# Kernel tuning notes

Measured on AMD Instinct MI355X. Metric: run time of the kernel, lower is better.

## Reference

```python
import jax, jax.numpy as jnp
import numpy as np

EPS = 1e-5


def layer_norm(x, g, b):
    m = jnp.mean(x, axis=-1, keepdims=True)
    v = jnp.mean((x - m) ** 2, axis=-1, keepdims=True)
    return (x - m) / jnp.sqrt(v + EPS) * g + b


def rel_shift(x, klen):
    # x: [q, p, b, n] -> Transformer-XL relative shift -> [q, klen, b, n]
    q, p, b, n = x.shape
    x = jnp.reshape(x, (p, q, b, n))
    x = x[1:]
    x = jnp.reshape(x, (q, p - 1, b, n))
    return x[:, :klen]


def setup_inputs() -> dict:
    S, B, D, NH, DH, DF = 1024, 4, 1024, 16, 64, 4096
    key = jax.random.key(0)
    ks = jax.random.split(key, 16)
    w = 0.02  # scale random params for numerical sanity
    return {
        "src": jax.random.normal(ks[0], (S, B, D), jnp.float32),
        "pos_emb": jax.random.normal(ks[1], (S + 1, B, D), jnp.float32),
        "src_mask": jnp.zeros((S, S), dtype=bool),
        "qw": jax.random.normal(ks[2], (D, NH, DH), jnp.float32) * w,
        "kw": jax.random.normal(ks[3], (D, NH, DH), jnp.float32) * w,
        "vw": jax.random.normal(ks[4], (D, NH, DH), jnp.float32) * w,
        "rw": jax.random.normal(ks[5], (D, NH, DH), jnp.float32) * w,
        "ow": jax.random.normal(ks[6], (D, NH, DH), jnp.float32) * w,
        "r_w_bias": jax.random.normal(ks[7], (NH, DH), jnp.float32) * w,
        "r_r_bias": jax.random.normal(ks[8], (NH, DH), jnp.float32) * w,
        "w1": jax.random.normal(ks[9], (DF, D), jnp.float32) * w,
        "b1": jnp.zeros((DF,), jnp.float32),
        "w2": jax.random.normal(ks[10], (D, DF), jnp.float32) * w,
        "b2": jnp.zeros((D,), jnp.float32),
        "g1": jnp.ones((D,), jnp.float32),
        "beta1": jnp.zeros((D,), jnp.float32),
        "g2": jnp.ones((D,), jnp.float32),
        "beta2": jnp.zeros((D,), jnp.float32),
    }


def reference(src, pos_emb, src_mask, qw, kw, vw, rw, ow, r_w_bias, r_r_bias,
              w1, b1, w2, b2, g1, beta1, g2, beta2):
    S = src.shape[0]
    d_head = qw.shape[-1]
    scale = 1.0 / d_head ** 0.5

    # mem=None -> cat == src; dropout layers are identity (eval)
    q_head = jnp.einsum('ibh,hnd->ibnd', src, qw)
    k_head = jnp.einsum('ibh,hnd->ibnd', src, kw)
    v_head = jnp.einsum('ibh,hnd->ibnd', src, vw)
    k_pos = jnp.einsum('ibh,hnd->ibnd', pos_emb, rw)

    ac = jnp.einsum('ibnd,jbnd->ijbn', q_head + r_w_bias, k_head)       # [S,S,B,N]
    bd = jnp.einsum('ibnd,jbnd->ijbn', q_head + r_r_bias, k_pos)        # [S,S+1,B,N]
    bd = rel_shift(bd, klen=S)

    mask = src_mask.astype(ac.dtype)[:, :, None, None]
    attn_score = (ac + bd) * scale - 1e30 * mask
    attn_prob = jax.nn.softmax(attn_score, axis=1)

    attn_vec = jnp.einsum('ijbn,jbnd->ibnd', attn_prob, v_head)
    attn_out = jnp.einsum('ibnd,hnd->ibh', attn_vec, ow)

    x = layer_norm(src + attn_out, g1, beta1)
    ff = jax.nn.gelu(x @ w1.T + b1, approximate=False) @ w2.T + b2
    return layer_norm(x + ff, g2, beta2)
```

## Files before the change

### kernel.cpp

```cpp
#include <hip/hip_runtime.h>
#include <math.h>

typedef __bf16 bf16x8 __attribute__((ext_vector_type(8)));
typedef __bf16 bf16x4 __attribute__((ext_vector_type(4)));
typedef float f32x4 __attribute__((ext_vector_type(4)));

__device__ __forceinline__ void gload_lds16(const __bf16* g, __bf16* l) {
  __builtin_amdgcn_global_load_lds((const __attribute__((address_space(1))) void*)g,
                                   (__attribute__((address_space(3))) void*)l, 16, 0, 0);
}

__device__ __forceinline__ float gelu_exact(float v) {
  return 0.5f * v * (1.f + erff(v * 0.70710678118654752f));
}

__global__ __launch_bounds__(256) void prep_all(
    const float* __restrict__ src, __bf16* __restrict__ srcB2,
    const float* __restrict__ pos, __bf16* __restrict__ posB,
    const float* __restrict__ ow, __bf16* __restrict__ owB,
    const float* __restrict__ w1, __bf16* __restrict__ w1B,
    const float* __restrict__ w2, __bf16* __restrict__ w2B,
    const float* __restrict__ qw, const float* __restrict__ kw,
    const float* __restrict__ vw, const float* __restrict__ rw,
    __bf16* __restrict__ qkvT, __bf16* __restrict__ rwT) {
  __shared__ float t[32][33];
  int bid = blockIdx.x;
  const int tid = threadIdx.x;
  if (bid < 4096) {
    const int i = bid & 1023, b = bid >> 10;
    const float4 v = *(const float4*)(src + ((size_t)(i * 4 + b)) * 1024 + tid * 4);
    bf16x4 o = {(__bf16)v.x, (__bf16)v.y, (__bf16)v.z, (__bf16)v.w};
    *(bf16x4*)(srcB2 + (size_t)bid * 1024 + tid * 4) = o;
    return;
  }
  bid -= 4096;
  if (bid < 3329) {
    const float* in; __bf16* out;
    if (bid < 1025) { in = pos; out = posB; }
    else if (bid < 1281) { bid -= 1025; in = ow; out = owB; }
    else if (bid < 2305) { bid -= 1281; in = w1; out = w1B; }
    else { bid -= 2305; in = w2; out = w2B; }
    const int base = bid * 4096 + tid * 4;
#pragma unroll
    for (int k2 = 0; k2 < 4; ++k2) {
      const int off = base + k2 * 1024;
      float4 v = *(const float4*)(in + off);
      bf16x4 o = {(__bf16)v.x, (__bf16)v.y, (__bf16)v.z, (__bf16)v.w};
      *(bf16x4*)(out + off) = o;
    }
    return;
  }
  bid -= 3329;
  const int z = bid >> 10, rem = bid & 1023;
  const float* in; __bf16* out;
  switch (z) {
    case 0: in = qw; out = qkvT; break;
    case 1: in = kw; out = qkvT + 1024 * 1024; break;
    case 2: in = vw; out = qkvT + 2048 * 1024; break;
    default: in = rw; out = rwT; break;
  }
  const int c0 = (rem & 31) * 32, r0 = (rem >> 5) * 32;
  const int tx = tid & 31, ty = tid >> 5;
  for (int yy = ty; yy < 32; yy += 8)
    t[yy][tx] = in[(size_t)(r0 + yy) * 1024 + c0 + tx];
  __syncthreads();
  for (int yy = ty; yy < 32; yy += 8)
    out[(size_t)(c0 + yy) * 1024 + r0 + tx] = (__bf16)t[tx][yy];
}

template<int BM, int BN, int MODE>
__device__ __forceinline__ void gemm_body(
    const __bf16* __restrict__ A, const __bf16* __restrict__ BT,
    float* __restrict__ Cf, __bf16* __restrict__ Cb,
    const float* __restrict__ bias, int M, int N, int K,
    int kStart, int kChunk, int mBase, int nBase, char* smemRaw) {
  constexpr int BK = 32;
  constexpr int ALOAD = (BM * BK) / 2048;
  constexpr int BLOAD = (BN * BK) / 2048;
  __bf16* lA = (__bf16*)smemRaw;
  __bf16* lB = (__bf16*)(smemRaw + 4 * BM * BK);
  const int tid = threadIdx.x;
  const int w = tid >> 6, l = tid & 63;
  const int lr = l & 15, lk = l >> 4;
  const int srow = tid >> 2;
  const int scol = (tid & 3) * 8;
  const int wbase = w * 512;

  const __bf16* aSrc[ALOAD];
  const __bf16* bSrc[BLOAD];
#pragma unroll
  for (int i = 0; i < ALOAD; ++i) {
    int grow = mBase + srow + i * 64;
    grow = grow < M ? grow : M - 1;
    aSrc[i] = A + (size_t)grow * K + kStart + scol;
  }
#pragma unroll
  for (int i = 0; i < BLOAD; ++i) {
    const int grow = nBase + srow + i * 64;
    bSrc[i] = BT + (size_t)grow * K + kStart + scol;
  }
  auto stage = [&](int buf) {
#pragma unroll
    for (int i = 0; i < ALOAD; ++i) {
      gload_lds16(aSrc[i], &lA[buf * BM * BK + i * 2048 + wbase]);
      aSrc[i] += BK;
    }
#pragma unroll
    for (int i = 0; i < BLOAD; ++i) {
      gload_lds16(bSrc[i], &lB[buf * BN * BK + i * 2048 + wbase]);
      bSrc[i] += BK;
    }
  };

  constexpr int WM = BM / 2, WN = BN / 2;
  constexpr int MF = WM / 16, NF = WN / 16;
  const int wr = w >> 1, wc = w & 1;
  f32x4 acc[MF][NF] = {};

  const int nIter = kChunk / BK;
  stage(0);
  int cur = 0;
#pragma unroll 1
  for (int t = 0; t < nIter; ++t) {
    __syncthreads();
    if (t + 1 < nIter) stage(cur ^ 1);
    bf16x8 af[MF], bfr[NF];
#pragma unroll
    for (int mi = 0; mi < MF; ++mi)
      af[mi] = *(const bf16x8*)&lA[cur * BM * BK + (wr * WM + mi * 16 + lr) * BK + lk * 8];
#pragma unroll
    for (int nj = 0; nj < NF; ++nj)
      bfr[nj] = *(const bf16x8*)&lB[cur * BN * BK + (wc * WN + nj * 16 + lr) * BK + lk * 8];
#pragma unroll
    for (int mi = 0; mi < MF; ++mi)
#pragma unroll
      for (int nj = 0; nj < NF; ++nj)
        acc[mi][nj] = __builtin_amdgcn_mfma_f32_16x16x32_bf16(af[mi], bfr[nj], acc[mi][nj], 0, 0, 0);
    cur ^= 1;
  }
#pragma unroll
  for (int mi = 0; mi < MF; ++mi) {
#pragma unroll
    for (int nj = 0; nj < NF; ++nj) {
      const int col = nBase + wc * WN + nj * 16 + lr;
      const int row0 = mBase + wr * WM + mi * 16 + lk * 4;
#pragma unroll
      for (int j = 0; j < 4; ++j) {
        const int row = row0 + j;
        if (row < M) {
          float v = acc[mi][nj][j];
          if constexpr (MODE == 1) {
            v = gelu_exact(v + bias[col]);
            Cb[(size_t)row * N + col] = (__bf16)v;
          } else if constexpr (MODE == 2) {
            Cb[(size_t)row * N + col] = (__bf16)v;
          } else {
            Cf[(size_t)row * N + col] = v;
          }
        }
      }
    }
  }
}

template<int BM, int BN, int MODE>
__global__ __launch_bounds__(256)
void gemm_bt(const __bf16* __restrict__ A, const __bf16* __restrict__ BT,
             float* __restrict__ Cf, float* __restrict__ Cf2,
             __bf16* __restrict__ Cb, const float* __restrict__ bias,
             int M, int N, int K, int kChunk) {
  __shared__ __align__(16) char smem[4 * (BM + BN) * 32];
  float* cf = (blockIdx.z == 1) ? Cf2 : Cf;
  const int gx = gridDim.x;
  const int G = gx * gridDim.y;
  const int flat = blockIdx.y * gx + blockIdx.x;
  const int swz = (flat & 7) * (G >> 3) + (flat >> 3);
  const int nx = swz % gx, ny = swz / gx;
  gemm_body<BM, BN, MODE>(A, BT, cf, Cb, bias, M, N, K, blockIdx.z * kChunk,
                          kChunk, ny * BM, nx * BN, smem);
}

__global__ __launch_bounds__(256)
void proj3_kernel(const __bf16* __restrict__ srcB2, const __bf16* __restrict__ qkvT,
                  const __bf16* __restrict__ vwT, const __bf16* __restrict__ posB,
                  const __bf16* __restrict__ rwT, __bf16* __restrict__ qkB,
                  __bf16* __restrict__ vTB, __bf16* __restrict__ kposB) {
  __shared__ __align__(16) char smem[4 * (128 + 64) * 32];
  const int raw = blockIdx.x;
  int bid = (raw & 7) * 258 + (raw >> 3);
  if (bid < 1024) {
    gemm_body<128, 64, 2>(srcB2, qkvT, nullptr, qkB, nullptr, 4096, 2048, 1024,
                          0, 1024, (bid >> 5) * 128, (bid & 31) * 64, smem);
  } else if (bid < 1536) {
    const int t = bid - 1024;
    gemm_body<128, 64, 2>(vwT, srcB2, nullptr, vTB, nullptr, 1024, 4096, 1024,
                          0, 1024, (t >> 6) * 128, (t & 63) * 64, smem);
  } else {
    const int t = bid - 1536;
    gemm_body<128, 64, 2>(posB, rwT, nullptr, kposB, nullptr, 4100, 1024, 1024,
                          0, 1024, (t >> 4) * 128, (t & 15) * 64, smem);
  }
}

__global__ __launch_bounds__(256)
void attn8(const __bf16* __restrict__ qk, const __bf16* __restrict__ vT,
           const __bf16* __restrict__ kpos, const float* __restrict__ rwbias,
           const float* __restrict__ rrbias, __bf16* __restrict__ av) {
  constexpr float ALPHA = 0.125f * 1.44269504088896f;
  constexpr int PB = 132;
  __shared__ __align__(16) char smem[74240];
  __bf16* sP  = (__bf16*)(smem + 49152);
  __bf16* sbd = (__bf16*)(smem + 57344);

  const int flat = blockIdx.x;
  const int xcd = flat & 7, rr_ = flat >> 3;
  const int bn = xcd * 8 + (rr_ >> 4);
  const int it = rr_ & 15;
  const int b = bn >> 4, n = bn & 15;
  const int i0 = it * 64;
  const int tid = threadIdx.x;
  const int l = tid & 63;
  const int lcol = l & 15, lk = l >> 4;
  const int strip = (tid >> 6) * 16;
  const int wbase = tid & 192;
  const int nh64 = n * 64;
  const int q = strip + lcol;

  const int rB = tid >> 3;
  const int cs8 = ((tid & 7) ^ (rB & 7)) * 8;

  bf16x8 onesf;
#pragma unroll
  for (int u = 0; u < 8; ++u) onesf[u] = (__bf16)1.0f;

  bf16x8 qac[2], qlo[2], qhi[2];
  {
    const __bf16* qrow = qk + ((size_t)(b * 1024 + i0 + q)) * 2048 + nh64;
    int gH = i0 + q + 1; gH = gH < 1024 ? gH : 1023;
    const __bf16* qrowH = qk + ((size_t)(b * 1024 + gH)) * 2048 + nh64;
#pragma unroll
    for (int kk = 0; kk < 2; ++kk) {
      bf16x8 qv = *(const bf16x8*)(qrow + kk * 32 + lk * 8);
      bf16x8 qh = *(const bf16x8*)(qrowH + kk * 32 + lk * 8);
      const int dbase = nh64 + kk * 32 + lk * 8;
#pragma unroll
      for (int u = 0; u < 8; ++u) {
        const float rb = rrbias[dbase + u];
        qac[kk][u] = (__bf16)(((float)qv[u] + rwbias[dbase + u]) * ALPHA);
        qlo[kk][u] = (__bf16)(((float)qv[u] + rb) * ALPHA);
        qhi[kk][u] = (__bf16)(((float)qh[u] + rb) * ALPHA);
      }
    }
  }

#pragma unroll
  for (int kq = 0; kq < 2; ++kq) {
    const int r = kq * 32 + rB;
    const int dst = (kq * 256 + wbase) * 8;
    gload_lds16(kpos + ((size_t)((960 - i0 + r) * 4 + b)) * 1024 + nh64 + cs8,
                (__bf16*)(smem + 40960) + dst);
    gload_lds16(qk + ((size_t)(b * 1024 + r)) * 2048 + 1024 + nh64 + cs8,
                (__bf16*)(smem) + dst);
    const int rrel = r - i0;
    const int idx = (rrel <= 0) ? (1024 + rrel) : (rrel - 1);
    gload_lds16(kpos + ((size_t)(idx * 4 + b)) * 1024 + nh64 + cs8,
                (__bf16*)(smem + 16384) + dst);
    gload_lds16(vT + ((size_t)(nh64 + r)) * 4096 + b * 1024 + cs8,
                (__bf16*)(smem + 32768) + dst);
  }
  __syncthreads();
  {
    __bf16* kpl = (__bf16*)(smem + 40960);
    const int colb0 = (-i0 - 64) & 127;
#pragma unroll
    for (int fb = 0; fb < 4; ++fb) {
      const int row = fb * 16 + lcol;
      f32x4 g = {};
#pragma unroll
      for (int kk = 0; kk < 2; ++kk) {
        bf16x8 a = *(const bf16x8*)&kpl[row * 64 + (((kk * 4 + lk) ^ (lcol & 7)) * 8)];
        g = __builtin_amdgcn_mfma_f32_16x16x32_bf16(a, qlo[kk], g, 0, 0, 0);
      }
      bf16x4 gw = {(__bf16)g[0], (__bf16)g[1], (__bf16)g[2], (__bf16)g[3]};
      *(bf16x4*)&sbd[q * PB + ((colb0 + fb * 16 + lk * 4) & 127)] = gw;
    }
  }
  __syncthreads();

  f32x4 oacc[4] = {};
  f32x4 zq = {};
  size_t kS = (size_t)(b * 1024 + 64 + rB) * 2048 + 1024 + nh64 + cs8;
  size_t vS = (size_t)(nh64 + rB) * 4096 + b * 1024 + 64 + cs8;

#pragma unroll 1
  for (int jt = 0; jt < 16; ++jt) {
    const int cur = jt & 1, nxt = cur ^ 1;
    const int d0 = jt * 64 - i0;
    __bf16* sK   = (__bf16*)(smem + cur * 8192);
    __bf16* sKn  = (__bf16*)(smem + nxt * 8192);
    __bf16* sKP  = (__bf16*)(smem + 16384 + cur * 8192);
    __bf16* sKPn = (__bf16*)(smem + 16384 + nxt * 8192);
    __bf16* sVT  = (__bf16*)(smem + 32768 + cur * 8192);
    __bf16* sVTn = (__bf16*)(smem + 32768 + nxt * 8192);
#pragma unroll
    for (int kq = 0; kq < 2; ++kq) {
      const int dst = (kq * 256 + wbase) * 8;
      gload_lds16(qk + kS + kq * 65536, sKn + dst);
      gload_lds16(vT + vS + kq * 131072, sVTn + dst);
      const int rreln = d0 + 64 + kq * 32 + rB;
      const int idx = (rreln <= 0) ? (1024 + rreln) : (rreln - 1);
      gload_lds16(kpos + ((size_t)(idx * 4 + b)) * 1024 + nh64 + cs8, sKPn + dst);
    }
    kS += 131072; vS += 64;
    {
      const bf16x8 qg0 = (d0 >= 0) ? qhi[0] : qlo[0];
      const bf16x8 qg1 = (d0 >= 0) ? qhi[1] : qlo[1];
#pragma unroll
      for (int fb = 0; fb < 4; ++fb) {
        const int row = fb * 16 + lcol;
        f32x4 g = {};
        g = __builtin_amdgcn_mfma_f32_16x16x32_bf16(
            *(const bf16x8*)&sKP[row * 64 + ((lk ^ (lcol & 7)) * 8)], qg0, g, 0, 0, 0);
        g = __builtin_amdgcn_mfma_f32_16x16x32_bf16(
            *(const bf16x8*)&sKP[row * 64 + (((4 + lk) ^ (lcol & 7)) * 8)], qg1, g, 0, 0, 0);
        bf16x4 gw = {(__bf16)g[0], (__bf16)g[1], (__bf16)g[2], (__bf16)g[3]};
        *(bf16x4*)&sbd[q * PB + ((d0 + fb * 16 + lk * 4) & 127)] = gw;
      }
      if (d0 == 0) {
        const int cl = tid >> 2, part = tid & 3;
        const __bf16* qs = qk + ((size_t)(b * 1024 + i0 + cl)) * 2048 + nh64 + part * 16;
        bf16x8 a0 = *(const bf16x8*)qs;
        bf16x8 a1 = *(const bf16x8*)(qs + 8);
        bf16x8 k0 = *(const bf16x8*)&sKP[(2 * part) * 8];
        bf16x8 k1 = *(const bf16x8*)&sKP[(2 * part + 1) * 8];
        float s64 = 0.f;
#pragma unroll
        for (int u = 0; u < 8; ++u)
          s64 += ((float)a0[u] + rrbias[nh64 + part * 16 + u]) * (float)k0[u]
               + ((float)a1[u] + rrbias[nh64 + part * 16 + 8 + u]) * (float)k1[u];
        s64 += __shfl_xor(s64, 1, 64);
        s64 += __shfl_xor(s64, 2, 64);
        if (part == 0) sbd[cl * PB] = (__bf16)(s64 * ALPHA);
      }
    }
    f32x4 sc[4];
#pragma unroll
    for (int fk = 0; fk < 4; ++fk) {
      const int row = fk * 16 + lcol;
      f32x4 a = {};
#pragma unroll
      for (int kk = 0; kk < 2; ++kk) {
        bf16x8 kf = *(const bf16x8*)&sK[row * 64 + (((kk * 4 + lk) ^ (lcol & 7)) * 8)];
        a = __builtin_amdgcn_mfma_f32_16x16x32_bf16(kf, qac[kk], a, 0, 0, 0);
      }
      sc[fk] = a;
    }
    {
      const int rowb = q * PB;
      const int sb = d0 - q;
#pragma unroll
      for (int fk = 0; fk < 4; ++fk) {
        const int cb = sb + fk * 16 + lk * 4;
        float e0 = exp2f(sc[fk][0] + (float)sbd[rowb + ((cb) & 127)]);
        float e1 = exp2f(sc[fk][1] + (float)sbd[rowb + ((cb + 1) & 127)]);
        float e2 = exp2f(sc[fk][2] + (float)sbd[rowb + ((cb + 2) & 127)]);
        float e3 = exp2f(sc[fk][3] + (float)sbd[rowb + ((cb + 3) & 127)]);
        bf16x4 pw = {(__bf16)e0, (__bf16)e1, (__bf16)e2, (__bf16)e3};
        *(bf16x4*)&sP[q * 64 + (((fk * 2 + (lk >> 1)) ^ (q & 7)) * 8) + (lk & 1) * 4] = pw;
      }
    }
#pragma unroll
    for (int kk = 0; kk < 2; ++kk) {
      bf16x8 pa = *(const bf16x8*)&sP[q * 64 + (((kk * 4 + lk) ^ (q & 7)) * 8)];
      zq = __builtin_amdgcn_mfma_f32_16x16x32_bf16(pa, onesf, zq, 0, 0, 0);
#pragma unroll
      for (int fd = 0; fd < 4; ++fd) {
        const int vrow = fd * 16 + lcol;
        bf16x8 bv = *(const bf16x8*)&sVT[vrow * 64 + (((kk * 4 + lk) ^ (lcol & 7)) * 8)];
        oacc[fd] = __builtin_amdgcn_mfma_f32_16x16x32_bf16(pa, bv, oacc[fd], 0, 0, 0);
      }
    }
    __syncthreads();
  }
#pragma unroll
  for (int jj = 0; jj < 4; ++jj) {
    const float rz = 1.f / zq[jj];
    const int ig = i0 + strip + lk * 4 + jj;
    __bf16* dst = av + ((size_t)(ig * 4 + b)) * 1024 + nh64;
#pragma unroll
    for (int fd = 0; fd < 4; ++fd)
      dst[fd * 16 + lcol] = (__bf16)(oacc[fd][jj] * rz);
  }
}

__global__ __launch_bounds__(256)
void ln_fuse(const float* __restrict__ A, const float* __restrict__ Bv,
             const float* __restrict__ Bv2, const float* __restrict__ cb,
             const float* __restrict__ g, const float* __restrict__ be,
             float* __restrict__ oF, __bf16* __restrict__ oB) {
  const int row = blockIdx.x, t = threadIdx.x;
  const size_t base = (size_t)row * 1024 + t * 4;
  const float4 a = *(const float4*)(A + base);
  const float4 bb = *(const float4*)(Bv + base);
  float x0 = a.x + bb.x, x1 = a.y + bb.y, x2 = a.z + bb.z, x3 = a.w + bb.w;
  if (Bv2) {
    const float4 c = *(const float4*)(Bv2 + base);
    x0 += c.x; x1 += c.y; x2 += c.z; x3 += c.w;
  }
  if (cb) {
    const float4 c = *(const float4*)(cb + t * 4);
    x0 += c.x; x1 += c.y; x2 += c.z; x3 += c.w;
  }
  float s = x0 + x1 + x2 + x3;
  float qq = x0 * x0 + x1 * x1 + x2 * x2 + x3 * x3;
#pragma unroll
  for (int o = 1; o < 64; o <<= 1) { s += __shfl_xor(s, o, 64); qq += __shfl_xor(qq, o, 64); }
  __shared__ float ss[4], qs[4];
  if ((t & 63) == 0) { ss[t >> 6] = s; qs[t >> 6] = qq; }
  __syncthreads();
  s = ss[0] + ss[1] + ss[2] + ss[3];
  qq = qs[0] + qs[1] + qs[2] + qs[3];
  const float mean = s * (1.f / 1024.f);
  const float var = qq * (1.f / 1024.f) - mean * mean;
  const float rstd = rsqrtf(var + 1e-5f);
  const float4 gv = *(const float4*)(g + t * 4);
  const float4 bev = *(const float4*)(be + t * 4);
  const float y0 = (x0 - mean) * rstd * gv.x + bev.x;
  const float y1 = (x1 - mean) * rstd * gv.y + bev.y;
  const float y2 = (x2 - mean) * rstd * gv.z + bev.z;
  const float y3 = (x3 - mean) * rstd * gv.w + bev.w;
  float4 r = {y0, y1, y2, y3};
  *(float4*)(oF + base) = r;
  if (oB) {
    bf16x4 o4 = {(__bf16)y0, (__bf16)y1, (__bf16)y2, (__bf16)y3};
    *(bf16x4*)(oB + base) = o4;
  }
}

extern "C" void kernel_launch(void* const* d_in, const int* in_sizes, int n_in,
                              void* d_out, int out_size, void* d_ws, size_t ws_size,
                              hipStream_t stream) {
  const float* src    = (const float*)d_in[0];
  const float* pos    = (const float*)d_in[1];
  const float* qw     = (const float*)d_in[3];
  const float* kw     = (const float*)d_in[4];
  const float* vw     = (const float*)d_in[5];
  const float* rw     = (const float*)d_in[6];
  const float* ow     = (const float*)d_in[7];
  const float* rwbias = (const float*)d_in[8];
  const float* rrbias = (const float*)d_in[9];
  const float* w1     = (const float*)d_in[10];
  const float* b1     = (const float*)d_in[11];
  const float* w2     = (const float*)d_in[12];
  const float* b2     = (const float*)d_in[13];
  const float* g1     = (const float*)d_in[14];
  const float* be1    = (const float*)d_in[15];
  const float* g2     = (const float*)d_in[16];
  const float* be2    = (const float*)d_in[17];
  float* out = (float*)d_out;

  char* p = (char*)d_ws;
  auto alloc = [&](size_t bytes) { char* r = p; p += (bytes + 255) & ~(size_t)255; return r; };
  __bf16* qkB   = (__bf16*)alloc(4096ull * 2048 * 2);
  __bf16* vTB   = (__bf16*)alloc(1024ull * 4096 * 2);
  __bf16* kposB = (__bf16*)alloc(4100ull * 1024 * 2);
  __bf16* avB   = (__bf16*)alloc(4096ull * 1024 * 2);
  __bf16* srcB2 = (__bf16*)alloc(4096ull * 1024 * 2);
  __bf16* posB  = (__bf16*)alloc(4100ull * 1024 * 2);
  float*  xF    = (float*)alloc(4096ull * 1024 * 4);
  __bf16* w2B   = (__bf16*)alloc(4096ull * 1024 * 2);
  __bf16* qkvT  = (__bf16*)alloc(3072ull * 1024 * 2);
  __bf16* rwT   = (__bf16*)alloc(1024ull * 1024 * 2);
  __bf16* owB   = (__bf16*)alloc(1024ull * 1024 * 2);
  __bf16* w1B   = (__bf16*)alloc(4096ull * 1024 * 2);
  __bf16* xB    = (__bf16*)alloc(4096ull * 1024 * 2);
  __bf16* gB  = qkB;
  float* aoP0 = (float*)srcB2;
  float* aoP1 = xF;
  float* ffP0 = (float*)avB;
  float* ffP1 = (float*)w1B;

  prep_all<<<11521, 256, 0, stream>>>(src, srcB2, pos, posB, ow, owB, w1, w1B,
                                      w2, w2B, qw, kw, vw, rw, qkvT, rwT);
  proj3_kernel<<<2064, 256, 0, stream>>>(srcB2, qkvT, qkvT + 2048 * 1024, posB,
                                         rwT, qkB, vTB, kposB);
  attn8<<<dim3(1024), 256, 0, stream>>>(qkB, vTB, kposB, rwbias, rrbias, avB);
  gemm_bt<128, 64, 0><<<dim3(16, 32, 2), 256, 0, stream>>>(avB, owB, aoP0, aoP1, nullptr, nullptr, 4096, 1024, 1024, 512);
  ln_fuse<<<4096, 256, 0, stream>>>(src, aoP0, aoP1, nullptr, g1, be1, xF, xB);
  gemm_bt<128, 64, 1><<<dim3(64, 32), 256, 0, stream>>>(xB, w1B, nullptr, nullptr, gB, b1, 4096, 4096, 1024, 1024);
  gemm_bt<128, 64, 0><<<dim3(16, 32, 2), 256, 0, stream>>>(gB, w2B, ffP0, ffP1, nullptr, nullptr, 4096, 1024, 4096, 2048);
  ln_fuse<<<4096, 256, 0, stream>>>(xF, ffP0, ffP1, b2, g2, be2, out, nullptr);
  (void)in_sizes; (void)n_in; (void)out_size; (void)ws_size;
}
```

Measured before the change: 330.1 us.

## Store split-K partial sums in bf16 and remap GEMM tile swizzle

The two split-K GEMMs (attention output projection and FFN down-projection) now write their partial results as bf16 instead of fp32, and the layernorm kernels read and sum bf16 partials. This halves the write and read traffic for the partial buffers. The block-to-tile swizzle is also changed so each group of eight consecutive blocks covers a band of rows and then walks columns, aiming for better L2 reuse. Rounding the partials to bf16 before the residual add and layernorm adds numerical error.

```diff
diff --git a/kernel.cpp b/kernel.cpp
--- a/kernel.cpp
+++ b/kernel.cpp
@@ -166,17 +166,20 @@
 template<int BM, int BN, int MODE>
 __global__ __launch_bounds__(256)
 void gemm_bt(const __bf16* __restrict__ A, const __bf16* __restrict__ BT,
-             float* __restrict__ Cf, float* __restrict__ Cf2,
-             __bf16* __restrict__ Cb, const float* __restrict__ bias,
+             float* __restrict__ Cf, __bf16* __restrict__ Cb,
+             __bf16* __restrict__ Cb2, const float* __restrict__ bias,
              int M, int N, int K, int kChunk) {
   __shared__ __align__(16) char smem[4 * (BM + BN) * 32];
-  float* cf = (blockIdx.z == 1) ? Cf2 : Cf;
+  __bf16* cb = (blockIdx.z == 1) ? Cb2 : Cb;
   const int gx = gridDim.x;
   const int G = gx * gridDim.y;
   const int flat = blockIdx.y * gx + blockIdx.x;
-  const int swz = (flat & 7) * (G >> 3) + (flat >> 3);
-  const int nx = swz % gx, ny = swz / gx;
-  gemm_body<BM, BN, MODE>(A, BT, cf, Cb, bias, M, N, K, blockIdx.z * kChunk,
+  const int band = G >> 3;
+  const int x8 = flat & 7, loc = flat >> 3;
+  const int rpb = band / gx;
+  const int ny = x8 * rpb + loc % rpb;
+  const int nx = loc / rpb;
+  gemm_body<BM, BN, MODE>(A, BT, Cf, cb, bias, M, N, K, blockIdx.z * kChunk,
                           kChunk, ny * BM, nx * BN, smem);
 }
 
@@ -394,19 +397,19 @@
 }
 
 __global__ __launch_bounds__(256)
-void ln_fuse(const float* __restrict__ A, const float* __restrict__ Bv,
-             const float* __restrict__ Bv2, const float* __restrict__ cb,
+void ln_fuse(const float* __restrict__ A, const __bf16* __restrict__ P0,
+             const __bf16* __restrict__ P1, const float* __restrict__ cb,
              const float* __restrict__ g, const float* __restrict__ be,
              float* __restrict__ oF, __bf16* __restrict__ oB) {
   const int row = blockIdx.x, t = threadIdx.x;
   const size_t base = (size_t)row * 1024 + t * 4;
   const float4 a = *(const float4*)(A + base);
-  const float4 bb = *(const float4*)(Bv + base);
-  float x0 = a.x + bb.x, x1 = a.y + bb.y, x2 = a.z + bb.z, x3 = a.w + bb.w;
-  if (Bv2) {
-    const float4 c = *(const float4*)(Bv2 + base);
-    x0 += c.x; x1 += c.y; x2 += c.z; x3 += c.w;
-  }
+  const bf16x4 p0 = *(const bf16x4*)(P0 + base);
+  const bf16x4 p1 = *(const bf16x4*)(P1 + base);
+  float x0 = a.x + (float)p0[0] + (float)p1[0];
+  float x1 = a.y + (float)p0[1] + (float)p1[1];
+  float x2 = a.z + (float)p0[2] + (float)p1[2];
+  float x3 = a.w + (float)p0[3] + (float)p1[3];
   if (cb) {
     const float4 c = *(const float4*)(cb + t * 4);
     x0 += c.x; x1 += c.y; x2 += c.z; x3 += c.w;
@@ -429,8 +432,10 @@
   const float y1 = (x1 - mean) * rstd * gv.y + bev.y;
   const float y2 = (x2 - mean) * rstd * gv.z + bev.z;
   const float y3 = (x3 - mean) * rstd * gv.w + bev.w;
-  float4 r = {y0, y1, y2, y3};
-  *(float4*)(oF + base) = r;
+  if (oF) {
+    float4 r = {y0, y1, y2, y3};
+    *(float4*)(oF + base) = r;
+  }
   if (oB) {
     bf16x4 o4 = {(__bf16)y0, (__bf16)y1, (__bf16)y2, (__bf16)y3};
     *(bf16x4*)(oB + base) = o4;
@@ -474,21 +479,21 @@
   __bf16* owB   = (__bf16*)alloc(1024ull * 1024 * 2);
   __bf16* w1B   = (__bf16*)alloc(4096ull * 1024 * 2);
   __bf16* xB    = (__bf16*)alloc(4096ull * 1024 * 2);
-  __bf16* gB  = qkB;
-  float* aoP0 = (float*)srcB2;
-  float* aoP1 = xF;
-  float* ffP0 = (float*)avB;
-  float* ffP1 = (float*)w1B;
+  __bf16* gB   = qkB;
+  __bf16* aoP0 = srcB2;
+  __bf16* aoP1 = posB;
+  __bf16* ffP0 = avB;
+  __bf16* ffP1 = w1B;
 
   prep_all<<<11521, 256, 0, stream>>>(src, srcB2, pos, posB, ow, owB, w1, w1B,
                                       w2, w2B, qw, kw, vw, rw, qkvT, rwT);
   proj3_kernel<<<2064, 256, 0, stream>>>(srcB2, qkvT, qkvT + 2048 * 1024, posB,
                                          rwT, qkB, vTB, kposB);
   attn8<<<dim3(1024), 256, 0, stream>>>(qkB, vTB, kposB, rwbias, rrbias, avB);
-  gemm_bt<128, 64, 0><<<dim3(16, 32, 2), 256, 0, stream>>>(avB, owB, aoP0, aoP1, nullptr, nullptr, 4096, 1024, 1024, 512);
+  gemm_bt<128, 64, 2><<<dim3(16, 32, 2), 256, 0, stream>>>(avB, owB, nullptr, aoP0, aoP1, nullptr, 4096, 1024, 1024, 512);
   ln_fuse<<<4096, 256, 0, stream>>>(src, aoP0, aoP1, nullptr, g1, be1, xF, xB);
-  gemm_bt<128, 64, 1><<<dim3(64, 32), 256, 0, stream>>>(xB, w1B, nullptr, nullptr, gB, b1, 4096, 4096, 1024, 1024);
-  gemm_bt<128, 64, 0><<<dim3(16, 32, 2), 256, 0, stream>>>(gB, w2B, ffP0, ffP1, nullptr, nullptr, 4096, 1024, 4096, 2048);
+  gemm_bt<128, 64, 1><<<dim3(64, 32), 256, 0, stream>>>(xB, w1B, nullptr, gB, nullptr, b1, 4096, 4096, 1024, 1024);
+  gemm_bt<128, 64, 2><<<dim3(16, 32, 2), 256, 0, stream>>>(gB, w2B, nullptr, ffP0, ffP1, nullptr, 4096, 1024, 4096, 2048);
   ln_fuse<<<4096, 256, 0, stream>>>(xF, ffP0, ffP1, b2, g2, be2, out, nullptr);
   (void)in_sizes; (void)n_in; (void)out_size; (void)ws_size;
 }
```

Measured after the change: 318.2 us. 3.6% less time.
